# Performance work log

Hardware: AMD Instinct MI355X
Metric: run time of the kernel (lower is better)

Reference implementation:

```python
import jax, jax.numpy as jnp
import numpy as np

N_NODES = 100000
N_EDGES = 200000  # per relation
D_NODE = 128
D_EDGE = 16
N_REL = 3  # agent-agent, agent-object, object-object


def setup_inputs() -> dict:
    key = jax.random.key(0)
    ks = jax.random.split(key, 6)
    x = jax.random.normal(ks[0], (N_NODES, D_NODE), dtype=jnp.float32)
    edge_attr = jax.random.normal(ks[1], (N_REL, N_EDGES, D_EDGE), dtype=jnp.float32)
    W_rel = jax.random.normal(ks[2], (N_REL, D_NODE, D_NODE), dtype=jnp.float32) / np.sqrt(D_NODE)
    We_rel = jax.random.normal(ks[3], (N_REL, D_EDGE, D_NODE), dtype=jnp.float32) / np.sqrt(D_EDGE)
    W_self = jax.random.normal(ks[4], (D_NODE, D_NODE), dtype=jnp.float32) / np.sqrt(D_NODE)
    b = jnp.zeros((D_NODE,), dtype=jnp.float32)
    edge_index = jax.random.randint(ks[5], (N_REL, N_EDGES, 2), 0, N_NODES, dtype=jnp.int32)
    return {"x": x, "edge_attr": edge_attr, "W_rel": W_rel, "We_rel": We_rel,
            "W_self": W_self, "b": b, "edge_index": edge_index}


def reference(x, edge_attr, W_rel, We_rel, W_self, b, edge_index):
    # Heterogeneous message passing: per relation r,
    #   msg_e = x[src_e] @ W_r + edge_attr_e @ We_r
    #   agg_r = scatter_add(msg, dst)
    # node update: relu(x @ W_self + sum_r agg_r + b)
    n = x.shape[0]
    src = edge_index[:, :, 0]  # [R, E]
    dst = edge_index[:, :, 1]  # [R, E]
    # gather source features per relation: [R, E, F]
    msgs = jnp.einsum('ref,rfo->reo', x[src], W_rel) \
         + jnp.einsum('reg,rgo->reo', edge_attr, We_rel)
    # scatter-add to destination nodes per relation -> [R, N, F]
    agg = jax.vmap(lambda m, d: jax.ops.segment_sum(m, d, num_segments=n))(msgs, dst)
    return jax.nn.relu(x @ W_self + agg.sum(axis=0) + b)
```

## Files before the change

kernel.cpp:

```cpp
#include <hip/hip_runtime.h>

#define NN 100000
#define NE 200000
#define DN 128
#define DE 16
#define NR 3
#define NEDGE (NR * NE)
#define NB1 98
#define NSTRIP 6250
#define GEMM_GRID 1024

typedef __attribute__((ext_vector_type(8))) short short8;
typedef __attribute__((ext_vector_type(4))) float f32x4;

__device__ __forceinline__ unsigned short f2bf(float f) {
    unsigned int u = __float_as_uint(f);
    u = (u + 0x7fffu + ((u >> 16) & 1u)) >> 16;
    return (unsigned short)u;
}

__global__ __launch_bounds__(256) void prep_kernel(
    const float* __restrict__ W_self, const float* __restrict__ W_rel,
    unsigned short* __restrict__ Wt,
    const int* __restrict__ ei, unsigned* __restrict__ cur,
    unsigned char* __restrict__ tmp)
{
    const int id = blockIdx.x * 256 + threadIdx.x;
    if (id < 65536) {
        const int m = id >> 14, rem = id & 16383;
        const int k = rem >> 7, n = rem & 127;
        const float* src = (m == 0) ? W_self : (W_rel + (size_t)(m - 1) * 16384);
        Wt[m * 16384 + n * 128 + k] = f2bf(src[k * 128 + n]);
    }
    const int2* ei2 = (const int2*)ei;
    for (int eid = id; eid < NEDGE; eid += 262144) {
        const int2 e = ei2[eid];
        const unsigned pos = atomicAdd(&cur[e.y], 1u);
        tmp[eid] = (unsigned char)pos;
    }
}

__global__ __launch_bounds__(256, 2) void gemm_kernel(
    const float* __restrict__ x,
    const unsigned short* __restrict__ Wt,
    unsigned short* __restrict__ zb,
    unsigned short* __restrict__ y)
{
    const int tid = threadIdx.x;
    const int m = tid >> 6;
    const int lane = tid & 63;
    const int lm = lane & 15;
    const int lq = lane >> 4;

    short8 bfr[8][4];
    {
        const unsigned short* wp = Wt + (size_t)m * 16384;
        #pragma unroll
        for (int cg = 0; cg < 8; ++cg)
            #pragma unroll
            for (int ks = 0; ks < 4; ++ks)
                bfr[cg][ks] = *(const short8*)(wp + (cg * 16 + lm) * 128 + ks * 32 + lq * 8);
    }
    unsigned short* outp = (m == 0) ? zb : (y + (size_t)(m - 1) * NN * 128);

    int s = blockIdx.x;
    float4 xb[8];
    {
        const float* xp = x + (size_t)(s * 16 + lm) * 128 + lq * 8;
        #pragma unroll
        for (int ks = 0; ks < 4; ++ks) {
            xb[2 * ks]     = *(const float4*)(xp + ks * 32);
            xb[2 * ks + 1] = *(const float4*)(xp + ks * 32 + 4);
        }
    }

    while (true) {
        short8 af[4];
        #pragma unroll
        for (int ks = 0; ks < 4; ++ks) {
            short8 t;
            t[0] = f2bf(xb[2 * ks].x);     t[1] = f2bf(xb[2 * ks].y);
            t[2] = f2bf(xb[2 * ks].z);     t[3] = f2bf(xb[2 * ks].w);
            t[4] = f2bf(xb[2 * ks + 1].x); t[5] = f2bf(xb[2 * ks + 1].y);
            t[6] = f2bf(xb[2 * ks + 1].z); t[7] = f2bf(xb[2 * ks + 1].w);
            af[ks] = t;
        }
        const int sn = s + GEMM_GRID;
        if (sn < NSTRIP) {
            const float* xp = x + (size_t)(sn * 16 + lm) * 128 + lq * 8;
            #pragma unroll
            for (int ks = 0; ks < 4; ++ks) {
                xb[2 * ks]     = *(const float4*)(xp + ks * 32);
                xb[2 * ks + 1] = *(const float4*)(xp + ks * 32 + 4);
            }
        }
        f32x4 acc[8];
        #pragma unroll
        for (int cg = 0; cg < 8; ++cg) acc[cg] = (f32x4){0.f, 0.f, 0.f, 0.f};
        #pragma unroll
        for (int cg = 0; cg < 8; ++cg)
            #pragma unroll
            for (int ks = 0; ks < 4; ++ks)
                acc[cg] = __builtin_amdgcn_mfma_f32_16x16x32_bf16(bfr[cg][ks], af[ks], acc[cg], 0, 0, 0);
        unsigned short* rp = outp + (size_t)(s * 16 + lm) * 128 + lq * 4;
        #pragma unroll
        for (int cg = 0; cg < 8; ++cg) {
            ushort4 o;
            o.x = f2bf(acc[cg][0]); o.y = f2bf(acc[cg][1]);
            o.z = f2bf(acc[cg][2]); o.w = f2bf(acc[cg][3]);
            *(ushort4*)(rp + cg * 16) = o;
        }
        if (sn >= NSTRIP) break;
        s = sn;
    }
}

__global__ __launch_bounds__(256) void scan1_kernel(
    const unsigned* __restrict__ cnt, unsigned* __restrict__ offs,
    unsigned* __restrict__ bsum)
{
    __shared__ unsigned wtot[4];
    const int tid = threadIdx.x, lane = tid & 63, wv = tid >> 6;
    const int base = blockIdx.x * 1024 + tid * 4;
    unsigned c[4];
    #pragma unroll
    for (int j = 0; j < 4; ++j) c[j] = (base + j < NN) ? cnt[base + j] : 0u;
    const unsigned ts = c[0] + c[1] + c[2] + c[3];
    unsigned incl = ts;
    #pragma unroll
    for (int d = 1; d < 64; d <<= 1) {
        unsigned v = __shfl_up(incl, d, 64);
        if (lane >= d) incl += v;
    }
    if (lane == 63) wtot[wv] = incl;
    __syncthreads();
    unsigned woff = 0;
    for (int p = 0; p < 4; ++p) if (p < wv) woff += wtot[p];
    unsigned run = woff + incl - ts;
    #pragma unroll
    for (int j = 0; j < 4; ++j) {
        if (base + j < NN) offs[base + j] = run;
        run += c[j];
    }
    if (tid == 255) bsum[blockIdx.x] = woff + incl;
}

__global__ void scan2_kernel(unsigned* __restrict__ bsum)
{
    const int lane = threadIdx.x;
    unsigned v[2], s = 0;
    const int base = lane * 2;
    #pragma unroll
    for (int j = 0; j < 2; ++j) {
        v[j] = (base + j < NB1) ? bsum[base + j] : 0u;
        s += v[j];
    }
    unsigned incl = s;
    #pragma unroll
    for (int d = 1; d < 64; d <<= 1) {
        unsigned t = __shfl_up(incl, d, 64);
        if (lane >= d) incl += t;
    }
    unsigned run = incl - s;
    #pragma unroll
    for (int j = 0; j < 2; ++j) {
        if (base + j < NB1) bsum[base + j] = run;
        run += v[j];
    }
}

__global__ __launch_bounds__(256) void scan3_kernel(
    unsigned* __restrict__ offs, const unsigned* __restrict__ bsum)
{
    const int base = blockIdx.x * 1024 + threadIdx.x * 4;
    const unsigned add = bsum[blockIdx.x];
    #pragma unroll
    for (int j = 0; j < 4; ++j)
        if (base + j < NN) offs[base + j] += add;
    if (blockIdx.x == 0 && threadIdx.x == 0) offs[NN] = NEDGE;
}

__global__ __launch_bounds__(256) void fill_kernel(
    const int* __restrict__ ei, const unsigned* __restrict__ offs,
    const unsigned char* __restrict__ tmp, uint2* __restrict__ elist)
{
    const int eid = blockIdx.x * 256 + threadIdx.x;
    if (eid < NEDGE) {
        const int2 e = ((const int2*)ei)[eid];
        const unsigned r = (eid >= 2 * NE) ? 2u : (eid >= NE ? 1u : 0u);
        const unsigned pos = offs[e.y] + (unsigned)tmp[eid];
        elist[pos] = make_uint2(r * NN + (unsigned)e.x, (unsigned)eid);
    }
}

__global__ __launch_bounds__(256) void aggregate_kernel(
    const unsigned short* __restrict__ zb,
    const unsigned short* __restrict__ y,
    const float* __restrict__ edge_attr,
    const float* __restrict__ We,
    const float* __restrict__ b,
    const unsigned* __restrict__ offs,
    const uint2* __restrict__ elist,
    float* __restrict__ out)
{
    const int tid = threadIdx.x;
    const int wv = tid >> 6, lane = tid & 63;
    const int dst0 = (blockIdx.x * 4 + wv) * 4;
    const int col = 2 * lane;
    const int k16 = lane & 15;

    unsigned sI[4], eI[4];
    #pragma unroll
    for (int d = 0; d < 4; ++d) {
        sI[d] = __builtin_amdgcn_readfirstlane(offs[dst0 + d]);
        eI[d] = __builtin_amdgcn_readfirstlane(offs[dst0 + d + 1]);
    }

    uint2 p[4][8];
    #pragma unroll
    for (int d = 0; d < 4; ++d) {
        const uint2* ep = elist + sI[d];
        #pragma unroll
        for (int j = 0; j < 8; ++j) {
            uint2 q = ep[j];
            q.x = (q.x < 3u * NN) ? q.x : 0u;
            q.y = (q.y < (unsigned)NEDGE) ? q.y : 0u;
            p[d][j] = q;
        }
    }

    float acc0[4], acc1[4], ea0[4], ea1[4], ea2[4];
    #pragma unroll
    for (int d = 0; d < 4; ++d) {
        const unsigned zv = *(const unsigned*)(zb + (size_t)(dst0 + d) * 128 + col);
        acc0[d] = __uint_as_float(zv << 16);
        acc1[d] = __uint_as_float(zv & 0xffff0000u);
        ea0[d] = 0.f; ea1[d] = 0.f; ea2[d] = 0.f;
    }

    unsigned v[4][8]; float a[4][8];
    #pragma unroll
    for (int d = 0; d < 4; ++d)
        #pragma unroll
        for (int j = 0; j < 8; ++j)
            v[d][j] = *(const unsigned*)(y + (size_t)p[d][j].x * 128 + col);
    #pragma unroll
    for (int d = 0; d < 4; ++d)
        #pragma unroll
        for (int j = 0; j < 8; ++j)
            a[d][j] = edge_attr[(size_t)p[d][j].y * 16 + k16];

    #pragma unroll
    for (int d = 0; d < 4; ++d)
        #pragma unroll
        for (int j = 0; j < 8; ++j) {
            const bool ok = (sI[d] + (unsigned)j) < eI[d];
            const unsigned vv = ok ? v[d][j] : 0u;
            const float aa = ok ? a[d][j] : 0.f;
            const unsigned py = p[d][j].y;
            acc0[d] += __uint_as_float(vv << 16);
            acc1[d] += __uint_as_float(vv & 0xffff0000u);
            ea0[d] += (py < NE) ? aa : 0.f;
            ea1[d] += (py >= NE && py < 2u * NE) ? aa : 0.f;
            ea2[d] += (py >= 2u * NE) ? aa : 0.f;
        }

    #pragma unroll
    for (int d = 0; d < 4; ++d)
        for (unsigned i = sI[d] + 8; i < eI[d]; ++i) {
            const uint2 q = elist[i];
            const unsigned vv = *(const unsigned*)(y + (size_t)q.x * 128 + col);
            const float aa = edge_attr[(size_t)q.y * 16 + k16];
            acc0[d] += __uint_as_float(vv << 16);
            acc1[d] += __uint_as_float(vv & 0xffff0000u);
            ea0[d] += (q.y < NE) ? aa : 0.f;
            ea1[d] += (q.y >= NE && q.y < 2u * NE) ? aa : 0.f;
            ea2[d] += (q.y >= 2u * NE) ? aa : 0.f;
        }

    #pragma unroll
    for (int k = 0; k < 16; ++k) {
        const float2 w0 = *(const float2*)(We + (0 * 16 + k) * 128 + col);
        const float2 w1 = *(const float2*)(We + (1 * 16 + k) * 128 + col);
        const float2 w2 = *(const float2*)(We + (2 * 16 + k) * 128 + col);
        #pragma unroll
        for (int d = 0; d < 4; ++d) {
            const float e0 = __uint_as_float((unsigned)__builtin_amdgcn_readlane((int)__float_as_uint(ea0[d]), k));
            const float e1 = __uint_as_float((unsigned)__builtin_amdgcn_readlane((int)__float_as_uint(ea1[d]), k));
            const float e2 = __uint_as_float((unsigned)__builtin_amdgcn_readlane((int)__float_as_uint(ea2[d]), k));
            acc0[d] = fmaf(e0, w0.x, acc0[d]);
            acc1[d] = fmaf(e0, w0.y, acc1[d]);
            acc0[d] = fmaf(e1, w1.x, acc0[d]);
            acc1[d] = fmaf(e1, w1.y, acc1[d]);
            acc0[d] = fmaf(e2, w2.x, acc0[d]);
            acc1[d] = fmaf(e2, w2.y, acc1[d]);
        }
    }

    const float2 bv = *(const float2*)(b + col);
    #pragma unroll
    for (int d = 0; d < 4; ++d) {
        float2 o;
        o.x = fmaxf(acc0[d] + bv.x, 0.f);
        o.y = fmaxf(acc1[d] + bv.y, 0.f);
        *(float2*)(out + (size_t)(dst0 + d) * 128 + col) = o;
    }
}

extern "C" void kernel_launch(void* const* d_in, const int* in_sizes, int n_in,
                              void* d_out, int out_size, void* d_ws, size_t ws_size,
                              hipStream_t stream)
{
    const float* x         = (const float*)d_in[0];
    const float* edge_attr = (const float*)d_in[1];
    const float* W_rel     = (const float*)d_in[2];
    const float* We_rel    = (const float*)d_in[3];
    const float* W_self    = (const float*)d_in[4];
    const float* b         = (const float*)d_in[5];
    const int*   edge_index= (const int*)d_in[6];
    float* out = (float*)d_out;

    char* wsb = (char*)d_ws;
    unsigned short* zb   = (unsigned short*)wsb;
    unsigned short* y    = (unsigned short*)(wsb + 25600000);
    unsigned short* Wt   = (unsigned short*)(wsb + 102400000);
    unsigned*       cur  = (unsigned*)(wsb + 102531072);
    unsigned*       offs = (unsigned*)(wsb + 102931072);
    unsigned*       bsum = (unsigned*)(wsb + 103331080);
    uint2*          elist= (uint2*)(wsb + 103331592);
    unsigned char*  tmp  = (unsigned char*)(wsb + 108131592);

    hipMemsetAsync(cur, 0, NN * sizeof(unsigned), stream);
    prep_kernel<<<1024, 256, 0, stream>>>(W_self, W_rel, Wt, edge_index, cur, tmp);
    gemm_kernel<<<GEMM_GRID, 256, 0, stream>>>(x, Wt, zb, y);

    scan1_kernel<<<NB1, 256, 0, stream>>>(cur, offs, bsum);
    scan2_kernel<<<1, 64, 0, stream>>>(bsum);
    scan3_kernel<<<NB1, 256, 0, stream>>>(offs, bsum);
    const int eblocks = (NEDGE + 255) / 256;
    fill_kernel <<<eblocks, 256, 0, stream>>>(edge_index, offs, tmp, elist);

    aggregate_kernel<<<NN / 16, 256, 0, stream>>>(zb, y, edge_attr, We_rel, b,
                                                  offs, elist, out);
}
```

Baseline: 306.8 us.

## Split edge-attribute projection into separate MFMA kernel and split edge list arrays

```diff
diff --git a/kernel.cpp b/kernel.cpp
--- a/kernel.cpp
+++ b/kernel.cpp
@@ -21,7 +21,8 @@
 
 __global__ __launch_bounds__(256) void prep_kernel(
     const float* __restrict__ W_self, const float* __restrict__ W_rel,
-    unsigned short* __restrict__ Wt,
+    const float* __restrict__ We,
+    unsigned short* __restrict__ Wt, unsigned short* __restrict__ Wea,
     const int* __restrict__ ei, unsigned* __restrict__ cur,
     unsigned char* __restrict__ tmp)
 {
@@ -31,6 +32,11 @@
         const int k = rem >> 7, n = rem & 127;
         const float* src = (m == 0) ? W_self : (W_rel + (size_t)(m - 1) * 16384);
         Wt[m * 16384 + n * 128 + k] = f2bf(src[k * 128 + n]);
+    } else if (id < 65536 + 8192) {
+        const int wid = id - 65536;
+        const int n = wid >> 6, k = wid & 63;
+        const float v = (k < 48) ? We[(k >> 4) * 2048 + (k & 15) * 128 + n] : 0.f;
+        Wea[n * 64 + k] = f2bf(v);
     }
     const int2* ei2 = (const int2*)ei;
     for (int eid = id; eid < NEDGE; eid += 262144) {
@@ -182,32 +188,99 @@
 
 __global__ __launch_bounds__(256) void fill_kernel(
     const int* __restrict__ ei, const unsigned* __restrict__ offs,
-    const unsigned char* __restrict__ tmp, uint2* __restrict__ elist)
+    const unsigned char* __restrict__ tmp,
+    unsigned* __restrict__ erow, unsigned* __restrict__ eeid)
 {
     const int eid = blockIdx.x * 256 + threadIdx.x;
     if (eid < NEDGE) {
         const int2 e = ((const int2*)ei)[eid];
         const unsigned r = (eid >= 2 * NE) ? 2u : (eid >= NE ? 1u : 0u);
         const unsigned pos = offs[e.y] + (unsigned)tmp[eid];
-        elist[pos] = make_uint2(r * NN + (unsigned)e.x, (unsigned)eid);
-    }
-}
-
-__global__ __launch_bounds__(256) void aggregate_kernel(
+        erow[pos] = r * NN + (unsigned)e.x;
+        eeid[pos] = (unsigned)eid;
+    }
+}
+
+__global__ __launch_bounds__(256, 4) void eaz_kernel(
+    const float* __restrict__ edge_attr,
+    const unsigned short* __restrict__ Wea,
+    const unsigned* __restrict__ offs,
+    const unsigned* __restrict__ eeid,
+    unsigned short* __restrict__ zb)
+{
+    __shared__ __align__(16) unsigned short eaS[16][64];
+    const int tid = threadIdx.x;
+    const int wv = tid >> 6, lane = tid & 63;
+    const int g = lane >> 4;
+    const int k16 = lane & 15;
+    const int row0 = blockIdx.x * 16;
+
+    #pragma unroll
+    for (int d = 0; d < 4; ++d) {
+        const int dst = row0 + wv * 4 + d;
+        const unsigned s = __builtin_amdgcn_readfirstlane(offs[dst]);
+        const unsigned e = __builtin_amdgcn_readfirstlane(offs[dst + 1]);
+        float ea = 0.f;
+        unsigned py[8];
+        #pragma unroll
+        for (int j = 0; j < 8; ++j) {
+            const unsigned q = eeid[s + j];
+            py[j] = (q < (unsigned)NEDGE) ? q : 0u;
+        }
+        float a[8];
+        #pragma unroll
+        for (int j = 0; j < 8; ++j)
+            a[j] = edge_attr[(size_t)py[j] * 16 + k16];
+        #pragma unroll
+        for (int j = 0; j < 8; ++j) {
+            const bool ok = ((s + (unsigned)j) < e)
+                && py[j] >= (unsigned)(g * NE) && py[j] < (unsigned)((g + 1) * NE);
+            ea += ok ? a[j] : 0.f;
+        }
+        for (unsigned i = s + 8; i < e; ++i) {
+            const unsigned q = eeid[i];
+            const float av = edge_attr[(size_t)q * 16 + k16];
+            const bool ok = q >= (unsigned)(g * NE) && q < (unsigned)((g + 1) * NE);
+            ea += ok ? av : 0.f;
+        }
+        eaS[wv * 4 + d][lane] = f2bf(ea);
+    }
+    __syncthreads();
+
+    const int lm = lane & 15, lq = lane >> 4;
+    const short8 af0 = *(const short8*)&eaS[lm][lq * 8];
+    const short8 af1 = *(const short8*)&eaS[lm][32 + lq * 8];
+    #pragma unroll
+    for (int h = 0; h < 2; ++h) {
+        const int cg = wv * 2 + h;
+        const short8 b0 = *(const short8*)(Wea + (cg * 16 + lm) * 64 + lq * 8);
+        const short8 b1 = *(const short8*)(Wea + (cg * 16 + lm) * 64 + 32 + lq * 8);
+        f32x4 acc = {0.f, 0.f, 0.f, 0.f};
+        acc = __builtin_amdgcn_mfma_f32_16x16x32_bf16(b0, af0, acc, 0, 0, 0);
+        acc = __builtin_amdgcn_mfma_f32_16x16x32_bf16(b1, af1, acc, 0, 0, 0);
+        unsigned short* zp = zb + (size_t)(row0 + lm) * 128 + cg * 16 + lq * 4;
+        const ushort4 old = *(const ushort4*)zp;
+        ushort4 o;
+        o.x = f2bf(__uint_as_float((unsigned)old.x << 16) + acc[0]);
+        o.y = f2bf(__uint_as_float((unsigned)old.y << 16) + acc[1]);
+        o.z = f2bf(__uint_as_float((unsigned)old.z << 16) + acc[2]);
+        o.w = f2bf(__uint_as_float((unsigned)old.w << 16) + acc[3]);
+        *(ushort4*)zp = o;
+    }
+}
+
+__global__ __launch_bounds__(256, 4) void aggregate_kernel(
     const unsigned short* __restrict__ zb,
     const unsigned short* __restrict__ y,
-    const float* __restrict__ edge_attr,
-    const float* __restrict__ We,
     const float* __restrict__ b,
     const unsigned* __restrict__ offs,
-    const uint2* __restrict__ elist,
+    const unsigned* __restrict__ erow,
     float* __restrict__ out)
 {
     const int tid = threadIdx.x;
     const int wv = tid >> 6, lane = tid & 63;
     const int dst0 = (blockIdx.x * 4 + wv) * 4;
     const int col = 2 * lane;
-    const int k16 = lane & 15;
 
     unsigned sI[4], eI[4];
     #pragma unroll
@@ -216,86 +289,47 @@
         eI[d] = __builtin_amdgcn_readfirstlane(offs[dst0 + d + 1]);
     }
 
-    uint2 p[4][8];
-    #pragma unroll
-    for (int d = 0; d < 4; ++d) {
-        const uint2* ep = elist + sI[d];
+    unsigned r[4][8];
+    #pragma unroll
+    for (int d = 0; d < 4; ++d) {
         #pragma unroll
         for (int j = 0; j < 8; ++j) {
-            uint2 q = ep[j];
-            q.x = (q.x < 3u * NN) ? q.x : 0u;
-            q.y = (q.y < (unsigned)NEDGE) ? q.y : 0u;
-            p[d][j] = q;
-        }
-    }
-
-    float acc0[4], acc1[4], ea0[4], ea1[4], ea2[4];
+            const unsigned q = erow[sI[d] + j];
+            r[d][j] = (q < 3u * NN) ? q : 0u;
+        }
+    }
+
+    unsigned v[4][8];
+    #pragma unroll
+    for (int d = 0; d < 4; ++d)
+        #pragma unroll
+        for (int j = 0; j < 8; ++j)
+            v[d][j] = *(const unsigned*)(y + (size_t)r[d][j] * 128 + col);
+
+    float acc0[4], acc1[4];
     #pragma unroll
     for (int d = 0; d < 4; ++d) {
         const unsigned zv = *(const unsigned*)(zb + (size_t)(dst0 + d) * 128 + col);
         acc0[d] = __uint_as_float(zv << 16);
         acc1[d] = __uint_as_float(zv & 0xffff0000u);
-        ea0[d] = 0.f; ea1[d] = 0.f; ea2[d] = 0.f;
-    }
-
-    unsigned v[4][8]; float a[4][8];
+    }
+
     #pragma unroll
     for (int d = 0; d < 4; ++d)
         #pragma unroll
-        for (int j = 0; j < 8; ++j)
-            v[d][j] = *(const unsigned*)(y + (size_t)p[d][j].x * 128 + col);
-    #pragma unroll
-    for (int d = 0; d < 4; ++d)
-        #pragma unroll
-        for (int j = 0; j < 8; ++j)
-            a[d][j] = edge_attr[(size_t)p[d][j].y * 16 + k16];
-
-    #pragma unroll
-    for (int d = 0; d < 4; ++d)
-        #pragma unroll
         for (int j = 0; j < 8; ++j) {
-            const bool ok = (sI[d] + (unsigned)j) < eI[d];
-            const unsigned vv = ok ? v[d][j] : 0u;
-            const float aa = ok ? a[d][j] : 0.f;
-            const unsigned py = p[d][j].y;
+            const unsigned vv = ((sI[d] + (unsigned)j) < eI[d]) ? v[d][j] : 0u;
             acc0[d] += __uint_as_float(vv << 16);
             acc1[d] += __uint_as_float(vv & 0xffff0000u);
-            ea0[d] += (py < NE) ? aa : 0.f;
-            ea1[d] += (py >= NE && py < 2u * NE) ? aa : 0.f;
-            ea2[d] += (py >= 2u * NE) ? aa : 0.f;
         }
 
     #pragma unroll
     for (int d = 0; d < 4; ++d)
         for (unsigned i = sI[d] + 8; i < eI[d]; ++i) {
-            const uint2 q = elist[i];
-            const unsigned vv = *(const unsigned*)(y + (size_t)q.x * 128 + col);
-            const float aa = edge_attr[(size_t)q.y * 16 + k16];
+            const unsigned vv = *(const unsigned*)(y + (size_t)erow[i] * 128 + col);
             acc0[d] += __uint_as_float(vv << 16);
             acc1[d] += __uint_as_float(vv & 0xffff0000u);
-            ea0[d] += (q.y < NE) ? aa : 0.f;
-            ea1[d] += (q.y >= NE && q.y < 2u * NE) ? aa : 0.f;
-            ea2[d] += (q.y >= 2u * NE) ? aa : 0.f;
-        }
-
-    #pragma unroll
-    for (int k = 0; k < 16; ++k) {
-        const float2 w0 = *(const float2*)(We + (0 * 16 + k) * 128 + col);
-        const float2 w1 = *(const float2*)(We + (1 * 16 + k) * 128 + col);
-        const float2 w2 = *(const float2*)(We + (2 * 16 + k) * 128 + col);
-        #pragma unroll
-        for (int d = 0; d < 4; ++d) {
-            const float e0 = __uint_as_float((unsigned)__builtin_amdgcn_readlane((int)__float_as_uint(ea0[d]), k));
-            const float e1 = __uint_as_float((unsigned)__builtin_amdgcn_readlane((int)__float_as_uint(ea1[d]), k));
-            const float e2 = __uint_as_float((unsigned)__builtin_amdgcn_readlane((int)__float_as_uint(ea2[d]), k));
-            acc0[d] = fmaf(e0, w0.x, acc0[d]);
-            acc1[d] = fmaf(e0, w0.y, acc1[d]);
-            acc0[d] = fmaf(e1, w1.x, acc0[d]);
-            acc1[d] = fmaf(e1, w1.y, acc1[d]);
-            acc0[d] = fmaf(e2, w2.x, acc0[d]);
-            acc1[d] = fmaf(e2, w2.y, acc1[d]);
-        }
-    }
+        }
 
     const float2 bv = *(const float2*)(b + col);
     #pragma unroll
@@ -324,22 +358,25 @@
     unsigned short* zb   = (unsigned short*)wsb;
     unsigned short* y    = (unsigned short*)(wsb + 25600000);
     unsigned short* Wt   = (unsigned short*)(wsb + 102400000);
-    unsigned*       cur  = (unsigned*)(wsb + 102531072);
-    unsigned*       offs = (unsigned*)(wsb + 102931072);
-    unsigned*       bsum = (unsigned*)(wsb + 103331080);
-    uint2*          elist= (uint2*)(wsb + 103331592);
-    unsigned char*  tmp  = (unsigned char*)(wsb + 108131592);
+    unsigned short* Wea  = (unsigned short*)(wsb + 102531072);
+    unsigned*       cur  = (unsigned*)(wsb + 102547456);
+    unsigned*       offs = (unsigned*)(wsb + 102947456);
+    unsigned*       bsum = (unsigned*)(wsb + 103347460);
+    unsigned*       erow = (unsigned*)(wsb + 103347972);
+    unsigned*       eeid = (unsigned*)(wsb + 105748004);
+    unsigned char*  tmp  = (unsigned char*)(wsb + 108148036);
 
     hipMemsetAsync(cur, 0, NN * sizeof(unsigned), stream);
-    prep_kernel<<<1024, 256, 0, stream>>>(W_self, W_rel, Wt, edge_index, cur, tmp);
+    prep_kernel<<<1024, 256, 0, stream>>>(W_self, W_rel, We_rel, Wt, Wea,
+                                          edge_index, cur, tmp);
     gemm_kernel<<<GEMM_GRID, 256, 0, stream>>>(x, Wt, zb, y);
 
     scan1_kernel<<<NB1, 256, 0, stream>>>(cur, offs, bsum);
     scan2_kernel<<<1, 64, 0, stream>>>(bsum);
     scan3_kernel<<<NB1, 256, 0, stream>>>(offs, bsum);
     const int eblocks = (NEDGE + 255) / 256;
-    fill_kernel <<<eblocks, 256, 0, stream>>>(edge_index, offs, tmp, elist);
-
-    aggregate_kernel<<<NN / 16, 256, 0, stream>>>(zb, y, edge_attr, We_rel, b,
-                                                  offs, elist, out);
-}
+    fill_kernel <<<eblocks, 256, 0, stream>>>(edge_index, offs, tmp, erow, eeid);
+
+    eaz_kernel<<<NN / 16, 256, 0, stream>>>(edge_attr, Wea, offs, eeid, zb);
+    aggregate_kernel<<<NN / 16, 256, 0, stream>>>(zb, y, b, offs, erow, out);
+}
```

After: 317.8 us. +3.6%, slower.
